# Performance work log

Hardware: AMD Instinct MI355X
Metric: run time of the kernel (lower is better)

Reference implementation:

```python
import jax, jax.numpy as jnp
import numpy as np

D_HIDDEN = 1024
D_MODEL = 1024
R_MIN, R_MAX = 0.0, 1.0
MAX_PHASE = 6.28
SEQ_LEN = 16384


def setup_inputs() -> dict:
    key = jax.random.key(0)
    k_in, k_th, k_nu, k_bre, k_bim, k_cre, k_cim, k_d = jax.random.split(key, 8)
    inputs = jax.random.normal(k_in, (SEQ_LEN, D_MODEL), dtype=jnp.float32)
    # theta_log ~ log(max_phase * U)
    u_th = jax.random.uniform(k_th, (D_HIDDEN,), dtype=jnp.float32)
    theta_log = jnp.log(MAX_PHASE * u_th)
    # nu_log ~ log(-0.5 * log(U*(r_max^2 - r_min^2) + r_min^2))
    u_nu = jax.random.uniform(k_nu, (D_HIDDEN,), dtype=jnp.float32)
    nu_log = jnp.log(-0.5 * jnp.log(u_nu * (R_MAX**2 - R_MIN**2) + R_MIN**2))
    # gamma_log = log(sqrt(1 - |lambda|^2))
    diag_lambda = jnp.exp(-jnp.exp(nu_log) + 1j * jnp.exp(theta_log))
    gamma_log = jnp.log(jnp.sqrt(1.0 - jnp.abs(diag_lambda) ** 2))
    norm_b = jnp.sqrt(2.0 * D_MODEL)
    norm_c = jnp.sqrt(1.0 * D_HIDDEN)
    B_re = jax.random.normal(k_bre, (D_HIDDEN, D_MODEL), dtype=jnp.float32) / norm_b
    B_im = jax.random.normal(k_bim, (D_HIDDEN, D_MODEL), dtype=jnp.float32) / norm_b
    C_re = jax.random.normal(k_cre, (D_MODEL, D_HIDDEN), dtype=jnp.float32) / norm_c
    C_im = jax.random.normal(k_cim, (D_MODEL, D_HIDDEN), dtype=jnp.float32) / norm_c
    Dp = jax.random.normal(k_d, (D_MODEL,), dtype=jnp.float32)
    return {"inputs": inputs, "nu_log": nu_log, "theta_log": theta_log,
            "gamma_log": gamma_log, "B_re": B_re, "B_im": B_im,
            "C_re": C_re, "C_im": C_im, "Dp": Dp}


def _binop(q_i, q_j):
    # elementwise associative op for diagonal linear recurrence
    A_i, b_i = q_i
    A_j, b_j = q_j
    return (A_j * A_i, A_j * b_i + b_j)


def reference(inputs, nu_log, theta_log, gamma_log, B_re, B_im, C_re, C_im, Dp):
    # diag_lambda: [H] complex64
    diag_lambda = jnp.exp(-jnp.exp(nu_log) + 1j * jnp.exp(theta_log))
    B_norm = (B_re + 1j * B_im) * jnp.exp(gamma_log)[:, None]  # [H, D]
    C = C_re + 1j * C_im                                        # [D, H]
    L = inputs.shape[0]
    # Bu_t = B_norm @ x_t  -> [L, H] complex
    Bu = inputs.astype(B_norm.dtype) @ B_norm.T
    Lambda = jnp.broadcast_to(diag_lambda[None, :], (L, diag_lambda.shape[0]))
    # parallel scan of h_t = lambda * h_{t-1} + Bu_t (initial state = 0)
    _, hidden = jax.lax.associative_scan(_binop, (Lambda, Bu))  # [L, H]
    # y_t = Re[C h_t] + D * x_t
    outputs = jnp.real(hidden @ C.T) + Dp * inputs              # [L, D]
    return (hidden[-1:], outputs)
```

## Files before the change

### kernel.cpp

```cpp
#include <hip/hip_runtime.h>
#include <stdint.h>
#include <stddef.h>

typedef __bf16 bf16;
typedef __attribute__((ext_vector_type(8))) __bf16 bf16x8;
typedef __attribute__((ext_vector_type(4))) __bf16 bf16x4;
typedef __attribute__((ext_vector_type(4))) float f32x4;

#define L_SEQ 16384
#define DH    1024
#define DM    1024
#define NC    256
#define LC    (L_SEQ / NC)

__device__ __forceinline__ void async_copy16(const void* g, void* l) {
  __builtin_amdgcn_global_load_lds((const __attribute__((address_space(1))) void*)g,
                                   (__attribute__((address_space(3))) void*)l,
                                   16, 0, 0);
}


__global__ void k_prep_params(const float* __restrict__ nu_log,
                              const float* __restrict__ theta_log,
                              const float* __restrict__ gamma_log,
                              float* __restrict__ lam_re, float* __restrict__ lam_im,
                              float* __restrict__ lamC_re, float* __restrict__ lamC_im,
                              float* __restrict__ gamma) {
  int h = blockIdx.x * blockDim.x + threadIdx.x;
  if (h >= DH) return;
  float nu  = expf(nu_log[h]);
  float th  = expf(theta_log[h]);
  float mag = expf(-nu);
  float lr = mag * cosf(th);
  float li = mag * sinf(th);
  lam_re[h] = lr; lam_im[h] = li;
  float ar = lr, ai = li;
#pragma unroll
  for (int i = 0; i < 6; ++i) {
    float nr = ar * ar - ai * ai;
    float ni = 2.f * ar * ai;
    ar = nr; ai = ni;
  }
  lamC_re[h] = ar; lamC_im[h] = ai;
  gamma[h] = expf(gamma_log[h]);
}

__global__ void k_cast_x(const float* __restrict__ x, bf16* __restrict__ xb) {
  int i = (blockIdx.x * blockDim.x + threadIdx.x) * 8;
  const float4 a = *(const float4*)(x + i);
  const float4 b = *(const float4*)(x + i + 4);
  bf16x8 v;
  v[0] = (bf16)a.x; v[1] = (bf16)a.y; v[2] = (bf16)a.z; v[3] = (bf16)a.w;
  v[4] = (bf16)b.x; v[5] = (bf16)b.y; v[6] = (bf16)b.z; v[7] = (bf16)b.w;
  *(bf16x8*)(xb + i) = v;
}

__global__ void k_prep_w(const float* __restrict__ B_re, const float* __restrict__ B_im,
                         const float* __restrict__ gamma, bf16* __restrict__ Wcat) {
  int idx = (blockIdx.x * blockDim.x + threadIdx.x) * 4;
  int h = idx / DM;
  int d = idx - h * DM;
  float g = gamma[h];
  float4 re = *(const float4*)(B_re + idx);
  float4 im = *(const float4*)(B_im + idx);
  bf16x4 vr, vi;
  vr[0] = (bf16)(re.x * g); vr[1] = (bf16)(re.y * g);
  vr[2] = (bf16)(re.z * g); vr[3] = (bf16)(re.w * g);
  vi[0] = (bf16)(im.x * g); vi[1] = (bf16)(im.y * g);
  vi[2] = (bf16)(im.z * g); vi[3] = (bf16)(im.w * g);
  *(bf16x4*)(Wcat + (size_t)h * DM + d)        = vr;
  *(bf16x4*)(Wcat + (size_t)(DH + h) * DM + d) = vi;
}

__global__ void k_prep_c(const float* __restrict__ C_re, const float* __restrict__ C_im,
                         bf16* __restrict__ Ccat) {
  int idx = (blockIdx.x * blockDim.x + threadIdx.x) * 4;
  int d = idx / DH;
  int k = idx - d * DH;
  float4 re = *(const float4*)(C_re + idx);
  float4 im = *(const float4*)(C_im + idx);
  bf16x4 vr, vi;
  vr[0] = (bf16)re.x; vr[1] = (bf16)re.y; vr[2] = (bf16)re.z; vr[3] = (bf16)re.w;
  vi[0] = (bf16)(-im.x); vi[1] = (bf16)(-im.y); vi[2] = (bf16)(-im.z); vi[3] = (bf16)(-im.w);
  *(bf16x4*)(Ccat + (size_t)d * (2 * DH) + k)      = vr;
  *(bf16x4*)(Ccat + (size_t)d * (2 * DH) + DH + k) = vi;
}

template <int MODE>
__global__ __launch_bounds__(256, 2)
void k_gemm(const bf16* __restrict__ A, const bf16* __restrict__ B,
            void* __restrict__ Cout, const float* __restrict__ x,
            const float* __restrict__ dp, int K, int N) {
  __shared__ bf16 As[128 * 64];
  __shared__ bf16 Bs[128 * 64];
  const int tid  = threadIdx.x;
  const int lane = tid & 63;
  const int wave = tid >> 6;
  const int wm = wave >> 1, wn = wave & 1;
  const int quad = lane >> 4;
  const int l16  = lane & 15;
  const int m0 = blockIdx.x * 128;
  const int n0 = blockIdx.y * 128;

  f32x4 acc[4][4];
#pragma unroll
  for (int i = 0; i < 4; ++i)
#pragma unroll
    for (int j = 0; j < 4; ++j)
      acc[i][j] = f32x4{0.f, 0.f, 0.f, 0.f};

  for (int k0 = 0; k0 < K; k0 += 64) {
    __syncthreads();
#pragma unroll
    for (int q = 0; q < 4; ++q) {
      const int c = q * 256 + tid;
      const int row = c >> 3, b = c & 7;
      async_copy16(A + (size_t)(m0 + row) * K + k0 + b * 8, (char*)As + c * 16);
      async_copy16(B + (size_t)(n0 + row) * K + k0 + b * 8, (char*)Bs + c * 16);
    }
    __syncthreads();
#pragma unroll
    for (int kk = 0; kk < 64; kk += 32) {
      bf16x8 fa[4], fb[4];
#pragma unroll
      for (int i = 0; i < 4; ++i) {
        fa[i] = *(const bf16x8*)(As + (wm * 64 + i * 16 + l16) * 64 + kk + quad * 8);
        fb[i] = *(const bf16x8*)(Bs + (wn * 64 + i * 16 + l16) * 64 + kk + quad * 8);
      }
#pragma unroll
      for (int i = 0; i < 4; ++i)
#pragma unroll
        for (int j = 0; j < 4; ++j)
          acc[i][j] = __builtin_amdgcn_mfma_f32_16x16x32_bf16(fa[i], fb[j], acc[i][j], 0, 0, 0);
    }
  }

  const int crow0 = m0 + wm * 64 + quad * 4;
  const int ccol0 = n0 + wn * 64 + l16;
  if (MODE == 0) {
    bf16* out = (bf16*)Cout;
#pragma unroll
    for (int i = 0; i < 4; ++i)
#pragma unroll
      for (int j = 0; j < 4; ++j)
#pragma unroll
        for (int p = 0; p < 4; ++p)
          out[(size_t)(crow0 + i * 16 + p) * N + ccol0 + j * 16] = (bf16)acc[i][j][p];
  } else {
    float* out = (float*)Cout;
#pragma unroll
    for (int j = 0; j < 4; ++j) {
      const int col = ccol0 + j * 16;
      const float dpv = dp[col];
#pragma unroll
      for (int i = 0; i < 4; ++i)
#pragma unroll
        for (int p = 0; p < 4; ++p) {
          const int row = crow0 + i * 16 + p;
          out[(size_t)row * N + col] = acc[i][j][p] + dpv * x[(size_t)row * N + col];
        }
    }
  }
}


__global__ void k_scan_local(const bf16* __restrict__ Bu,
                             const float* __restrict__ lam_re,
                             const float* __restrict__ lam_im,
                             float* __restrict__ chunk_end) {
  const int h = blockIdx.y * 256 + threadIdx.x;
  const int c = blockIdx.x;
  const float lr = lam_re[h], li = lam_im[h];
  float hr = 0.f, hi = 0.f;
  const bf16* p = Bu + (size_t)c * LC * (2 * DH) + h;
#pragma unroll 4
  for (int t = 0; t < LC; ++t) {
    float br = (float)p[0];
    float bi = (float)p[DH];
    float nr = lr * hr - li * hi + br;
    float ni = lr * hi + li * hr + bi;
    hr = nr; hi = ni;
    p += 2 * DH;
  }
  chunk_end[(size_t)c * (2 * DH) + h]      = hr;
  chunk_end[(size_t)c * (2 * DH) + DH + h] = hi;
}

__global__ void k_scan_chunks(const float* __restrict__ chunk_end,
                              const float* __restrict__ lamC_re,
                              const float* __restrict__ lamC_im,
                              float* __restrict__ carry_in,
                              float* __restrict__ out_final,
                              int interleave) {
  const int h = blockIdx.x * 256 + threadIdx.x;
  const float lr = lamC_re[h], li = lamC_im[h];
  float er = 0.f, ei = 0.f;
  for (int c = 0; c < NC; ++c) {
    carry_in[(size_t)c * (2 * DH) + h]      = er;
    carry_in[(size_t)c * (2 * DH) + DH + h] = ei;
    float cr = chunk_end[(size_t)c * (2 * DH) + h];
    float ci = chunk_end[(size_t)c * (2 * DH) + DH + h];
    float nr = lr * er - li * ei + cr;
    float ni = lr * ei + li * er + ci;
    er = nr; ei = ni;
  }
  if (interleave) {
    out_final[2 * h]     = er;
    out_final[2 * h + 1] = ei;
  } else {
    out_final[h] = er;
  }
}

__global__ void k_scan_apply(bf16* __restrict__ Bu,
                             const float* __restrict__ lam_re,
                             const float* __restrict__ lam_im,
                             const float* __restrict__ carry_in) {
  const int h = blockIdx.y * 256 + threadIdx.x;
  const int c = blockIdx.x;
  const float lr = lam_re[h], li = lam_im[h];
  float hr = carry_in[(size_t)c * (2 * DH) + h];
  float hi = carry_in[(size_t)c * (2 * DH) + DH + h];
  bf16* p = Bu + (size_t)c * LC * (2 * DH) + h;
#pragma unroll 4
  for (int t = 0; t < LC; ++t) {
    float br = (float)p[0];
    float bi = (float)p[DH];
    float nr = lr * hr - li * hi + br;
    float ni = lr * hi + li * hr + bi;
    hr = nr; hi = ni;
    p[0]  = (bf16)hr;
    p[DH] = (bf16)hi;
    p += 2 * DH;
  }
}


extern "C" void kernel_launch(void* const* d_in, const int* in_sizes, int n_in,
                              void* d_out, int out_size, void* d_ws, size_t ws_size,
                              hipStream_t stream) {
  const float* inputs    = (const float*)d_in[0];
  const float* nu_log    = (const float*)d_in[1];
  const float* theta_log = (const float*)d_in[2];
  const float* gamma_log = (const float*)d_in[3];
  const float* B_re      = (const float*)d_in[4];
  const float* B_im      = (const float*)d_in[5];
  const float* C_re      = (const float*)d_in[6];
  const float* C_im      = (const float*)d_in[7];
  const float* Dp        = (const float*)d_in[8];

  char* ws = (char*)d_ws;
  float* lam_re    = (float*)(ws + 0);
  float* lam_im    = (float*)(ws + 4096);
  float* lamC_re   = (float*)(ws + 8192);
  float* lamC_im   = (float*)(ws + 12288);
  float* gamma     = (float*)(ws + 16384);
  float* chunk_end = (float*)(ws + 65536);
  float* carry_in  = (float*)(ws + 65536 + (2u << 20));
  bf16*  Wcat      = (bf16*) (ws + 65536 + (4u << 20));
  bf16*  Ccat      = (bf16*) (ws + 65536 + (8u << 20));
  bf16*  Xb        = (bf16*) (ws + 65536 + (12u << 20));
  bf16*  Bu        = (bf16*) (ws + 65536 + (44u << 20));

  int interleave = 1;
  int state_floats = 2048;
  if (out_size == 1024 + L_SEQ * DM) { interleave = 0; state_floats = 1024; }

  float* out_state = (float*)d_out;
  float* out_y     = (float*)d_out + state_floats;

  k_prep_params<<<dim3(4), dim3(256), 0, stream>>>(nu_log, theta_log, gamma_log,
                                                   lam_re, lam_im, lamC_re, lamC_im, gamma);
  k_cast_x<<<dim3((L_SEQ * DM) / 8 / 256), dim3(256), 0, stream>>>(inputs, Xb);
  k_prep_w<<<dim3((DH * DM) / 4 / 256), dim3(256), 0, stream>>>(B_re, B_im, gamma, Wcat);
  k_prep_c<<<dim3((DM * DH) / 4 / 256), dim3(256), 0, stream>>>(C_re, C_im, Ccat);

  k_gemm<0><<<dim3(L_SEQ / 128, (2 * DH) / 128), dim3(256), 0, stream>>>(
      Xb, Wcat, (void*)Bu, nullptr, nullptr, DM, 2 * DH);

  k_scan_local<<<dim3(NC, DH / 256), dim3(256), 0, stream>>>(Bu, lam_re, lam_im, chunk_end);
  k_scan_chunks<<<dim3(DH / 256), dim3(256), 0, stream>>>(chunk_end, lamC_re, lamC_im,
                                                          carry_in, out_state, interleave);
  k_scan_apply<<<dim3(NC, DH / 256), dim3(256), 0, stream>>>(Bu, lam_re, lam_im, carry_in);

  k_gemm<1><<<dim3(L_SEQ / 128, DM / 128), dim3(256), 0, stream>>>(
      Bu, Ccat, (void*)out_y, inputs, Dp, 2 * DH, DM);

  (void)in_sizes; (void)n_in; (void)ws_size;
}
```

Before: 414.2 us.

## Swizzle GEMM LDS layout, fuse prep kernels, and vectorize scan passes

XOR-swizzles the 16-byte slots of the GEMM shared-memory tiles to cut LDS bank conflicts on the MFMA fragment reads, and raises the launch-bounds occupancy hint from 2 to 3. The cast and weight-prep kernels are merged into one launch, with gamma computed inline. The scan kernels now handle two hidden channels per thread using bf16x2 loads and stores, and use an interleaved re/im layout for chunk_end and carry_in so those accesses are vectorized. The occupancy hint can force register spilling given the 64 f32 accumulators per thread, and the scan kernels now launch half as many threads, which reduces parallelism.

```diff
diff --git a/kernel.cpp b/kernel.cpp
--- a/kernel.cpp
+++ b/kernel.cpp
@@ -5,7 +5,9 @@
 typedef __bf16 bf16;
 typedef __attribute__((ext_vector_type(8))) __bf16 bf16x8;
 typedef __attribute__((ext_vector_type(4))) __bf16 bf16x4;
+typedef __attribute__((ext_vector_type(2))) __bf16 bf16x2;
 typedef __attribute__((ext_vector_type(4))) float f32x4;
+typedef __attribute__((ext_vector_type(2))) float f32x2;
 
 #define L_SEQ 16384
 #define DH    1024
@@ -22,10 +24,8 @@
 
 __global__ void k_prep_params(const float* __restrict__ nu_log,
                               const float* __restrict__ theta_log,
-                              const float* __restrict__ gamma_log,
                               float* __restrict__ lam_re, float* __restrict__ lam_im,
-                              float* __restrict__ lamC_re, float* __restrict__ lamC_im,
-                              float* __restrict__ gamma) {
+                              float* __restrict__ lamC_re, float* __restrict__ lamC_im) {
   int h = blockIdx.x * blockDim.x + threadIdx.x;
   if (h >= DH) return;
   float nu  = expf(nu_log[h]);
@@ -42,52 +42,54 @@
     ar = nr; ai = ni;
   }
   lamC_re[h] = ar; lamC_im[h] = ai;
-  gamma[h] = expf(gamma_log[h]);
-}
-
-__global__ void k_cast_x(const float* __restrict__ x, bf16* __restrict__ xb) {
-  int i = (blockIdx.x * blockDim.x + threadIdx.x) * 8;
-  const float4 a = *(const float4*)(x + i);
-  const float4 b = *(const float4*)(x + i + 4);
-  bf16x8 v;
-  v[0] = (bf16)a.x; v[1] = (bf16)a.y; v[2] = (bf16)a.z; v[3] = (bf16)a.w;
-  v[4] = (bf16)b.x; v[5] = (bf16)b.y; v[6] = (bf16)b.z; v[7] = (bf16)b.w;
-  *(bf16x8*)(xb + i) = v;
-}
-
-__global__ void k_prep_w(const float* __restrict__ B_re, const float* __restrict__ B_im,
-                         const float* __restrict__ gamma, bf16* __restrict__ Wcat) {
-  int idx = (blockIdx.x * blockDim.x + threadIdx.x) * 4;
-  int h = idx / DM;
-  int d = idx - h * DM;
-  float g = gamma[h];
-  float4 re = *(const float4*)(B_re + idx);
-  float4 im = *(const float4*)(B_im + idx);
-  bf16x4 vr, vi;
-  vr[0] = (bf16)(re.x * g); vr[1] = (bf16)(re.y * g);
-  vr[2] = (bf16)(re.z * g); vr[3] = (bf16)(re.w * g);
-  vi[0] = (bf16)(im.x * g); vi[1] = (bf16)(im.y * g);
-  vi[2] = (bf16)(im.z * g); vi[3] = (bf16)(im.w * g);
-  *(bf16x4*)(Wcat + (size_t)h * DM + d)        = vr;
-  *(bf16x4*)(Wcat + (size_t)(DH + h) * DM + d) = vi;
-}
-
-__global__ void k_prep_c(const float* __restrict__ C_re, const float* __restrict__ C_im,
-                         bf16* __restrict__ Ccat) {
-  int idx = (blockIdx.x * blockDim.x + threadIdx.x) * 4;
-  int d = idx / DH;
-  int k = idx - d * DH;
-  float4 re = *(const float4*)(C_re + idx);
-  float4 im = *(const float4*)(C_im + idx);
-  bf16x4 vr, vi;
-  vr[0] = (bf16)re.x; vr[1] = (bf16)re.y; vr[2] = (bf16)re.z; vr[3] = (bf16)re.w;
-  vi[0] = (bf16)(-im.x); vi[1] = (bf16)(-im.y); vi[2] = (bf16)(-im.z); vi[3] = (bf16)(-im.w);
-  *(bf16x4*)(Ccat + (size_t)d * (2 * DH) + k)      = vr;
-  *(bf16x4*)(Ccat + (size_t)d * (2 * DH) + DH + k) = vi;
+}
+
+#define NB_CAST 8192
+#define NB_W    1024
+__global__ void k_prep_all(const float* __restrict__ x, bf16* __restrict__ xb,
+                           const float* __restrict__ B_re, const float* __restrict__ B_im,
+                           const float* __restrict__ gamma_log, bf16* __restrict__ Wcat,
+                           const float* __restrict__ C_re, const float* __restrict__ C_im,
+                           bf16* __restrict__ Ccat) {
+  const int b = blockIdx.x;
+  if (b < NB_CAST) {
+    int i = (b * 256 + (int)threadIdx.x) * 8;
+    const float4 a0 = *(const float4*)(x + i);
+    const float4 a1 = *(const float4*)(x + i + 4);
+    bf16x8 v;
+    v[0] = (bf16)a0.x; v[1] = (bf16)a0.y; v[2] = (bf16)a0.z; v[3] = (bf16)a0.w;
+    v[4] = (bf16)a1.x; v[5] = (bf16)a1.y; v[6] = (bf16)a1.z; v[7] = (bf16)a1.w;
+    *(bf16x8*)(xb + i) = v;
+  } else if (b < NB_CAST + NB_W) {
+    int idx = ((b - NB_CAST) * 256 + (int)threadIdx.x) * 4;
+    int h = idx / DM;
+    int d = idx - h * DM;
+    float g = expf(gamma_log[h]);
+    float4 re = *(const float4*)(B_re + idx);
+    float4 im = *(const float4*)(B_im + idx);
+    bf16x4 vr, vi;
+    vr[0] = (bf16)(re.x * g); vr[1] = (bf16)(re.y * g);
+    vr[2] = (bf16)(re.z * g); vr[3] = (bf16)(re.w * g);
+    vi[0] = (bf16)(im.x * g); vi[1] = (bf16)(im.y * g);
+    vi[2] = (bf16)(im.z * g); vi[3] = (bf16)(im.w * g);
+    *(bf16x4*)(Wcat + (size_t)h * DM + d)        = vr;
+    *(bf16x4*)(Wcat + (size_t)(DH + h) * DM + d) = vi;
+  } else {
+    int idx = ((b - NB_CAST - NB_W) * 256 + (int)threadIdx.x) * 4;
+    int d = idx / DH;
+    int k = idx - d * DH;
+    float4 re = *(const float4*)(C_re + idx);
+    float4 im = *(const float4*)(C_im + idx);
+    bf16x4 vr, vi;
+    vr[0] = (bf16)re.x; vr[1] = (bf16)re.y; vr[2] = (bf16)re.z; vr[3] = (bf16)re.w;
+    vi[0] = (bf16)(-im.x); vi[1] = (bf16)(-im.y); vi[2] = (bf16)(-im.z); vi[3] = (bf16)(-im.w);
+    *(bf16x4*)(Ccat + (size_t)d * (2 * DH) + k)      = vr;
+    *(bf16x4*)(Ccat + (size_t)d * (2 * DH) + DH + k) = vi;
+  }
 }
 
 template <int MODE>
-__global__ __launch_bounds__(256, 2)
+__global__ __launch_bounds__(256, 3)
 void k_gemm(const bf16* __restrict__ A, const bf16* __restrict__ B,
             void* __restrict__ Cout, const float* __restrict__ x,
             const float* __restrict__ dp, int K, int N) {
@@ -114,18 +116,24 @@
 #pragma unroll
     for (int q = 0; q < 4; ++q) {
       const int c = q * 256 + tid;
-      const int row = c >> 3, b = c & 7;
-      async_copy16(A + (size_t)(m0 + row) * K + k0 + b * 8, (char*)As + c * 16);
-      async_copy16(B + (size_t)(n0 + row) * K + k0 + b * 8, (char*)Bs + c * 16);
+      const int row = c >> 3, slot = c & 7;
+      const int part = slot ^ (row & 7);
+      async_copy16(A + (size_t)(m0 + row) * K + k0 + part * 8, (char*)As + c * 16);
+      async_copy16(B + (size_t)(n0 + row) * K + k0 + part * 8, (char*)Bs + c * 16);
     }
     __syncthreads();
 #pragma unroll
     for (int kk = 0; kk < 64; kk += 32) {
+      const int pbase = (kk >> 3);
       bf16x8 fa[4], fb[4];
 #pragma unroll
       for (int i = 0; i < 4; ++i) {
-        fa[i] = *(const bf16x8*)(As + (wm * 64 + i * 16 + l16) * 64 + kk + quad * 8);
-        fb[i] = *(const bf16x8*)(Bs + (wn * 64 + i * 16 + l16) * 64 + kk + quad * 8);
+        const int ra = wm * 64 + i * 16 + l16;
+        const int rb = wn * 64 + i * 16 + l16;
+        const int sa = (pbase + quad) ^ (ra & 7);
+        const int sb = (pbase + quad) ^ (rb & 7);
+        fa[i] = *(const bf16x8*)(As + ra * 64 + sa * 8);
+        fb[i] = *(const bf16x8*)(Bs + rb * 64 + sb * 8);
       }
 #pragma unroll
       for (int i = 0; i < 4; ++i)
@@ -168,22 +176,24 @@
                              const float* __restrict__ lam_re,
                              const float* __restrict__ lam_im,
                              float* __restrict__ chunk_end) {
-  const int h = blockIdx.y * 256 + threadIdx.x;
+  const int h2 = (blockIdx.y * 256 + threadIdx.x) * 2;
   const int c = blockIdx.x;
-  const float lr = lam_re[h], li = lam_im[h];
-  float hr = 0.f, hi = 0.f;
-  const bf16* p = Bu + (size_t)c * LC * (2 * DH) + h;
+  const float lr0 = lam_re[h2],     li0 = lam_im[h2];
+  const float lr1 = lam_re[h2 + 1], li1 = lam_im[h2 + 1];
+  float hr0 = 0.f, hi0 = 0.f, hr1 = 0.f, hi1 = 0.f;
+  const bf16* p = Bu + (size_t)c * LC * (2 * DH) + h2;
 #pragma unroll 4
   for (int t = 0; t < LC; ++t) {
-    float br = (float)p[0];
-    float bi = (float)p[DH];
-    float nr = lr * hr - li * hi + br;
-    float ni = lr * hi + li * hr + bi;
-    hr = nr; hi = ni;
+    bf16x2 br = *(const bf16x2*)(p);
+    bf16x2 bi = *(const bf16x2*)(p + DH);
+    float nr0 = lr0 * hr0 - li0 * hi0 + (float)br[0];
+    float ni0 = lr0 * hi0 + li0 * hr0 + (float)bi[0];
+    float nr1 = lr1 * hr1 - li1 * hi1 + (float)br[1];
+    float ni1 = lr1 * hi1 + li1 * hr1 + (float)bi[1];
+    hr0 = nr0; hi0 = ni0; hr1 = nr1; hi1 = ni1;
     p += 2 * DH;
   }
-  chunk_end[(size_t)c * (2 * DH) + h]      = hr;
-  chunk_end[(size_t)c * (2 * DH) + DH + h] = hi;
+  *(f32x4*)(chunk_end + (size_t)c * (2 * DH) + 2 * h2) = f32x4{hr0, hi0, hr1, hi1};
 }
 
 __global__ void k_scan_chunks(const float* __restrict__ chunk_end,
@@ -195,13 +205,12 @@
   const int h = blockIdx.x * 256 + threadIdx.x;
   const float lr = lamC_re[h], li = lamC_im[h];
   float er = 0.f, ei = 0.f;
+#pragma unroll 16
   for (int c = 0; c < NC; ++c) {
-    carry_in[(size_t)c * (2 * DH) + h]      = er;
-    carry_in[(size_t)c * (2 * DH) + DH + h] = ei;
-    float cr = chunk_end[(size_t)c * (2 * DH) + h];
-    float ci = chunk_end[(size_t)c * (2 * DH) + DH + h];
-    float nr = lr * er - li * ei + cr;
-    float ni = lr * ei + li * er + ci;
+    *(f32x2*)(carry_in + (size_t)c * (2 * DH) + 2 * h) = f32x2{er, ei};
+    f32x2 ce = *(const f32x2*)(chunk_end + (size_t)c * (2 * DH) + 2 * h);
+    float nr = lr * er - li * ei + ce[0];
+    float ni = lr * ei + li * er + ce[1];
     er = nr; ei = ni;
   }
   if (interleave) {
@@ -216,21 +225,27 @@
                              const float* __restrict__ lam_re,
                              const float* __restrict__ lam_im,
                              const float* __restrict__ carry_in) {
-  const int h = blockIdx.y * 256 + threadIdx.x;
+  const int h2 = (blockIdx.y * 256 + threadIdx.x) * 2;
   const int c = blockIdx.x;
-  const float lr = lam_re[h], li = lam_im[h];
-  float hr = carry_in[(size_t)c * (2 * DH) + h];
-  float hi = carry_in[(size_t)c * (2 * DH) + DH + h];
-  bf16* p = Bu + (size_t)c * LC * (2 * DH) + h;
+  const float lr0 = lam_re[h2],     li0 = lam_im[h2];
+  const float lr1 = lam_re[h2 + 1], li1 = lam_im[h2 + 1];
+  f32x4 cv = *(const f32x4*)(carry_in + (size_t)c * (2 * DH) + 2 * h2);
+  float hr0 = cv[0], hi0 = cv[1], hr1 = cv[2], hi1 = cv[3];
+  bf16* p = Bu + (size_t)c * LC * (2 * DH) + h2;
 #pragma unroll 4
   for (int t = 0; t < LC; ++t) {
-    float br = (float)p[0];
-    float bi = (float)p[DH];
-    float nr = lr * hr - li * hi + br;
-    float ni = lr * hi + li * hr + bi;
-    hr = nr; hi = ni;
-    p[0]  = (bf16)hr;
-    p[DH] = (bf16)hi;
+    bf16x2 br = *(const bf16x2*)(p);
+    bf16x2 bi = *(const bf16x2*)(p + DH);
+    float nr0 = lr0 * hr0 - li0 * hi0 + (float)br[0];
+    float ni0 = lr0 * hi0 + li0 * hr0 + (float)bi[0];
+    float nr1 = lr1 * hr1 - li1 * hi1 + (float)br[1];
+    float ni1 = lr1 * hi1 + li1 * hr1 + (float)bi[1];
+    hr0 = nr0; hi0 = ni0; hr1 = nr1; hi1 = ni1;
+    bf16x2 wr, wi;
+    wr[0] = (bf16)hr0; wr[1] = (bf16)hr1;
+    wi[0] = (bf16)hi0; wi[1] = (bf16)hi1;
+    *(bf16x2*)(p)      = wr;
+    *(bf16x2*)(p + DH) = wi;
     p += 2 * DH;
   }
 }
@@ -254,7 +269,6 @@
   float* lam_im    = (float*)(ws + 4096);
   float* lamC_re   = (float*)(ws + 8192);
   float* lamC_im   = (float*)(ws + 12288);
-  float* gamma     = (float*)(ws + 16384);
   float* chunk_end = (float*)(ws + 65536);
   float* carry_in  = (float*)(ws + 65536 + (2u << 20));
   bf16*  Wcat      = (bf16*) (ws + 65536 + (4u << 20));
@@ -269,19 +283,18 @@
   float* out_state = (float*)d_out;
   float* out_y     = (float*)d_out + state_floats;
 
-  k_prep_params<<<dim3(4), dim3(256), 0, stream>>>(nu_log, theta_log, gamma_log,
-                                                   lam_re, lam_im, lamC_re, lamC_im, gamma);
-  k_cast_x<<<dim3((L_SEQ * DM) / 8 / 256), dim3(256), 0, stream>>>(inputs, Xb);
-  k_prep_w<<<dim3((DH * DM) / 4 / 256), dim3(256), 0, stream>>>(B_re, B_im, gamma, Wcat);
-  k_prep_c<<<dim3((DM * DH) / 4 / 256), dim3(256), 0, stream>>>(C_re, C_im, Ccat);
+  k_prep_params<<<dim3(4), dim3(256), 0, stream>>>(nu_log, theta_log,
+                                                   lam_re, lam_im, lamC_re, lamC_im);
+  k_prep_all<<<dim3(NB_CAST + 2 * NB_W), dim3(256), 0, stream>>>(
+      inputs, Xb, B_re, B_im, gamma_log, Wcat, C_re, C_im, Ccat);
 
   k_gemm<0><<<dim3(L_SEQ / 128, (2 * DH) / 128), dim3(256), 0, stream>>>(
       Xb, Wcat, (void*)Bu, nullptr, nullptr, DM, 2 * DH);
 
-  k_scan_local<<<dim3(NC, DH / 256), dim3(256), 0, stream>>>(Bu, lam_re, lam_im, chunk_end);
-  k_scan_chunks<<<dim3(DH / 256), dim3(256), 0, stream>>>(chunk_end, lamC_re, lamC_im,
-                                                          carry_in, out_state, interleave);
-  k_scan_apply<<<dim3(NC, DH / 256), dim3(256), 0, stream>>>(Bu, lam_re, lam_im, carry_in);
+  k_scan_local<<<dim3(NC, 2), dim3(256), 0, stream>>>(Bu, lam_re, lam_im, chunk_end);
+  k_scan_chunks<<<dim3(4), dim3(256), 0, stream>>>(chunk_end, lamC_re, lamC_im,
+                                                   carry_in, out_state, interleave);
+  k_scan_apply<<<dim3(NC, 2), dim3(256), 0, stream>>>(Bu, lam_re, lam_im, carry_in);
 
   k_gemm<1><<<dim3(L_SEQ / 128, DM / 128), dim3(256), 0, stream>>>(
       Bu, Ccat, (void*)out_y, inputs, Dp, 2 * DH, DM);
```

New measurement: 396.3 us. 4.3% less time.
